# Kernel optimization log

Measured on AMD Instinct MI355X. Metric: run time of the kernel, lower is better.

Reference implementation:

```python
import jax, jax.numpy as jnp
import numpy as np

B, S, D, H = 2, 2048, 1024, 16
DK = D // H  # 64

def setup_inputs() -> dict:
    key = jax.random.key(0)
    ks = jax.random.split(key, 12)
    scale = 1.0 / np.sqrt(D)
    return {
        "q": jax.random.normal(ks[0], (B, S, D), jnp.float32),
        "k": jax.random.normal(ks[1], (B, S, D), jnp.float32),
        "v": jax.random.normal(ks[2], (B, S, D), jnp.float32),
        "Wq": jax.random.normal(ks[3], (D, D), jnp.float32) * scale,
        "bq": jnp.zeros((D,), jnp.float32),
        "Wk": jax.random.normal(ks[4], (D, D), jnp.float32) * scale,
        "bk": jnp.zeros((D,), jnp.float32),
        "Wv": jax.random.normal(ks[5], (D, D), jnp.float32) * scale,
        "bv": jnp.zeros((D,), jnp.float32),
        "Wo": jax.random.normal(ks[6], (D, D), jnp.float32) * scale,
        "bo": jnp.zeros((D,), jnp.float32),
        "mask": jnp.ones((B, 1, S, S), jnp.bool_),
    }

def reference(q, k, v, Wq, bq, Wk, bk, Wv, bv, Wo, bo, mask):
    # Linear projections: y = x @ W^T + b (torch nn.Linear convention)
    def proj(x, W, b):
        return x @ W.T + b
    # [B,S,D] -> [B,H,S,DK]
    def split_heads(x):
        return x.reshape(B, S, H, DK).transpose(0, 2, 1, 3)

    query = split_heads(proj(q, Wq, bq))
    key_ = split_heads(proj(k, Wk, bk))
    value = split_heads(proj(v, Wv, bv))

    # NOTE: original uses out-of-place masked_fill whose result is discarded,
    # so mask has no effect on the computation (reproduced faithfully here).
    scores = jnp.einsum('bhqd,bhkd->bhqk', query, key_) / jnp.sqrt(
        jnp.asarray(DK, query.dtype))
    attn = jax.nn.softmax(scores, axis=-1)  # dropout p=0.0: identity
    x = jnp.einsum('bhqk,bhkd->bhqd', attn, value)
    x = x.transpose(0, 2, 1, 3).reshape(B, S, D)
    return proj(x, Wo, bo)
```

## Files before the change

### kernel.cpp

```cpp
#include <hip/hip_runtime.h>
#include <hip/hip_bf16.h>


typedef __attribute__((ext_vector_type(8))) short bf16x8;
typedef __attribute__((ext_vector_type(4))) float f32x4;
typedef unsigned short u16;
typedef unsigned int u32;

#define MFMA16(a, b, c) __builtin_amdgcn_mfma_f32_16x16x32_bf16(a, b, c, 0, 0, 0)
#define EXP2(x) __builtin_amdgcn_exp2f(x)

static __device__ __forceinline__ u16 f2bf(float f) {
    union { __hip_bfloat16 h; u16 u; } v;
    v.h = __float2bfloat16(f);
    return v.u;
}

static __device__ __forceinline__ u16 f2bf_fast(float f) {
    return (u16)((__float_as_uint(f) + 0x8000u) >> 16);
}

static __device__ __forceinline__ void gload16(const u16* g, u16* l) {
    __builtin_amdgcn_global_load_lds(
        (const __attribute__((address_space(1))) void*)g,
        (__attribute__((address_space(3))) void*)l, 16, 0, 0);
}

static __device__ __forceinline__ void cvt16(float4 f0, float4 f1,
                                             float4 f2, float4 f3, u16* o) {
    o[0]=f2bf(f0.x);  o[1]=f2bf(f0.y);  o[2]=f2bf(f0.z);  o[3]=f2bf(f0.w);
    o[4]=f2bf(f1.x);  o[5]=f2bf(f1.y);  o[6]=f2bf(f1.z);  o[7]=f2bf(f1.w);
    o[8]=f2bf(f2.x);  o[9]=f2bf(f2.y);  o[10]=f2bf(f2.z); o[11]=f2bf(f2.w);
    o[12]=f2bf(f3.x); o[13]=f2bf(f3.y); o[14]=f2bf(f3.z); o[15]=f2bf(f3.w);
}

struct CvtArgs16 { const float* in[16]; u16* out[16]; };

__global__ __launch_bounds__(256)
void cvt_multi(CvtArgs16 a)
{
    const int tsel = blockIdx.x >> 9;
    const int i = (((blockIdx.x & 511) * 256) + threadIdx.x) * 8;
    const float* in = a.in[tsel];
    u16* out = a.out[tsel];
    float4 x = *(const float4*)(in + i);
    float4 y = *(const float4*)(in + i + 4);
    u16 o[8];
    o[0]=f2bf(x.x); o[1]=f2bf(x.y); o[2]=f2bf(x.z); o[3]=f2bf(x.w);
    o[4]=f2bf(y.x); o[5]=f2bf(y.y); o[6]=f2bf(y.z); o[7]=f2bf(y.w);
    *(uint4*)(out + i) = *(uint4*)o;
}

struct GemmArgs {
    const float* F[3]; const u16* Wb[3]; const float* bias[3];
    u16* C[3]; float osc[3]; int epi[3];
};

__global__ __launch_bounds__(256)
void gemm_qkv(GemmArgs g)
{
    __shared__ u16 lds_a[2][128 * 32];
    __shared__ u16 lds_b[2][128 * 32];

    const int z = blockIdx.y;
    const float* Fp = g.F[z];
    const u16*  Gp = g.Wb[z];
    const int epi = g.epi[z];

    const int t    = threadIdx.x;
    const int lane = t & 63;
    const int w    = t >> 6;
    const int wm   = w >> 1, wn = w & 1;
    const int ll   = lane & 15;
    const int lg   = lane >> 4;

    const int bx  = blockIdx.x;
    const int swz = (bx & 7) * 32 + (bx >> 3);
    const int tile_m = (epi == 1 ? (swz & 7) : (swz >> 3)) * 128;
    const int tile_n = (epi == 1 ? (swz >> 3) : (swz & 7)) * 128;

    const int rowF = (epi == 1) ? tile_n : tile_m;
    const int rowG = (epi == 1) ? tile_m : tile_n;

    const int c0   = w * 2;
    const int lrow = lane >> 2;
    const int lcol = (lane & 3) * 8;

    const int srow = t >> 1;
    const int scol = (t & 1) * 16;
    const float* Fbase = Fp + (size_t)(rowF + srow) * 1024 + scol;
    const u16*   Gb0   = Gp + (size_t)(rowG + c0 * 16 + lrow) * 1024 + lcol;

    f32x4 acc[4][4] = {};

    {
        u16* ldsG = (epi == 1) ? lds_a[0] : lds_b[0];
        #pragma unroll
        for (int j = 0; j < 2; j++)
            gload16(Gb0 + (size_t)j * 16 * 1024, &ldsG[(c0 + j) * 512]);

        float4 f0 = *(const float4*)(Fbase);
        float4 f1 = *(const float4*)(Fbase + 4);
        float4 f2 = *(const float4*)(Fbase + 8);
        float4 f3 = *(const float4*)(Fbase + 12);
        u16 tmp[16];
        cvt16(f0, f1, f2, f3, tmp);
        u16* ldsF = (epi == 1) ? lds_b[0] : lds_a[0];
        *(uint4*)&ldsF[srow * 32 + scol]     = *(uint4*)tmp;
        *(uint4*)&ldsF[srow * 32 + scol + 8] = *(uint4*)(tmp + 8);
    }
    __syncthreads();

    int cur = 0;
    for (int kt = 0; kt < 1024; kt += 32) {
        const int nxt = cur ^ 1;
        const bool more = (kt + 32 < 1024);

        float4 f0, f1, f2, f3;
        if (more) {
            const float* Fs = Fbase + kt + 32;
            f0 = *(const float4*)(Fs);
            f1 = *(const float4*)(Fs + 4);
            f2 = *(const float4*)(Fs + 8);
            f3 = *(const float4*)(Fs + 12);
            u16* ldsG = (epi == 1) ? lds_a[nxt] : lds_b[nxt];
            #pragma unroll
            for (int j = 0; j < 2; j++)
                gload16(Gb0 + (size_t)j * 16 * 1024 + kt + 32,
                        &ldsG[(c0 + j) * 512]);
        }

        bf16x8 af[4], bfr[4];
        #pragma unroll
        for (int i = 0; i < 4; i++)
            af[i] = *(bf16x8*)&lds_a[cur][(wm * 64 + i * 16 + ll) * 32 + lg * 8];
        #pragma unroll
        for (int j = 0; j < 4; j++)
            bfr[j] = *(bf16x8*)&lds_b[cur][(wn * 64 + j * 16 + ll) * 32 + lg * 8];
        #pragma unroll
        for (int i = 0; i < 4; i++)
            #pragma unroll
            for (int j = 0; j < 4; j++)
                acc[i][j] = MFMA16(af[i], bfr[j], acc[i][j]);

        if (more) {
            u16 tmp[16];
            cvt16(f0, f1, f2, f3, tmp);
            u16* ldsF = (epi == 1) ? lds_b[nxt] : lds_a[nxt];
            *(uint4*)&ldsF[srow * 32 + scol]     = *(uint4*)tmp;
            *(uint4*)&ldsF[srow * 32 + scol + 8] = *(uint4*)(tmp + 8);
        }

        __syncthreads();
        cur = nxt;
    }

    const float osc = g.osc[z];
    const float* bias = g.bias[z];
    u16* Cp = g.C[z];

    #pragma unroll
    for (int i = 0; i < 4; i++) {
        const int row0 = tile_m + wm * 64 + i * 16 + lg * 4;
        #pragma unroll
        for (int j = 0; j < 4; j++) {
            const int col = tile_n + wn * 64 + j * 16 + ll;
            if (epi == 1) {
                const int b = col >> 11, s = col & 2047;
                #pragma unroll
                for (int r = 0; r < 4; r++)
                    Cp[(size_t)(b * 1024 + row0 + r) * 2048 + s] =
                        f2bf(acc[i][j][r] + bias[row0 + r]);
            } else {
                const float bias_v = bias[col];
                const int h = col >> 6, dk = col & 63;
                const int b = row0 >> 11;
                #pragma unroll
                for (int r = 0; r < 4; r++) {
                    const int s = (row0 + r) & 2047;
                    Cp[((size_t)(b * 16 + h) * 2048 + s) * 64 + dk] =
                        f2bf((acc[i][j][r] + bias_v) * osc);
                }
            }
        }
    }
}

__global__ __launch_bounds__(256)
void gemm_out(const u16* __restrict__ Ap, const u16* __restrict__ Wp,
              const float* __restrict__ bias, float* __restrict__ Cp)
{
    __shared__ u16 lds_a[2][128 * 32];
    __shared__ u16 lds_b[2][64 * 32];

    const int t    = threadIdx.x;
    const int lane = t & 63;
    const int w    = t >> 6;
    const int wm   = w >> 1, wn = w & 1;
    const int ll   = lane & 15;
    const int lg   = lane >> 4;

    const int bx  = blockIdx.x;
    const int swz = (bx & 7) * 64 + (bx >> 3);
    const int tile_m = (swz >> 4) * 128;
    const int tile_n = (swz & 15) * 64;

    const int lrow = lane >> 2;
    const int lcol = (lane & 3) * 8;

    f32x4 acc[4][2] = {};

    #define OSTAGE(buf, kt)                                                    \
    {                                                                          \
        _Pragma("unroll")                                                      \
        for (int j = 0; j < 3; j++) {                                          \
            const int c = w * 3 + j;                                           \
            if (c < 8) {                                                       \
                const int row = tile_m + c * 16 + lrow;                        \
                const int col = (kt) + lcol;                                   \
                const u16* ga = Ap + ((size_t)((row >> 11) * 16 + (col >> 6))  \
                                      * 2048 + (row & 2047)) * 64 + (col & 63);\
                gload16(ga, &lds_a[buf][c * 512]);                             \
            } else {                                                           \
                const int cc = c - 8;                                          \
                gload16(Wp + (size_t)(tile_n + cc * 16 + lrow) * 1024          \
                        + (kt) + lcol, &lds_b[buf][cc * 512]);                 \
            }                                                                  \
        }                                                                      \
    }

    OSTAGE(0, 0);
    __syncthreads();

    int cur = 0;
    for (int kt = 0; kt < 1024; kt += 32) {
        if (kt + 32 < 1024) OSTAGE(cur ^ 1, kt + 32);

        bf16x8 af[4], bfr[2];
        #pragma unroll
        for (int i = 0; i < 4; i++)
            af[i] = *(bf16x8*)&lds_a[cur][(wm * 64 + i * 16 + ll) * 32 + lg * 8];
        #pragma unroll
        for (int j = 0; j < 2; j++)
            bfr[j] = *(bf16x8*)&lds_b[cur][(wn * 32 + j * 16 + ll) * 32 + lg * 8];
        #pragma unroll
        for (int i = 0; i < 4; i++)
            #pragma unroll
            for (int j = 0; j < 2; j++)
                acc[i][j] = MFMA16(af[i], bfr[j], acc[i][j]);

        __syncthreads();
        cur ^= 1;
    }
    #undef OSTAGE

    #pragma unroll
    for (int i = 0; i < 4; i++) {
        const int row0 = tile_m + wm * 64 + i * 16 + lg * 4;
        #pragma unroll
        for (int j = 0; j < 2; j++) {
            const int col = tile_n + wn * 32 + j * 16 + ll;
            const float bias_v = bias[col];
            #pragma unroll
            for (int r = 0; r < 4; r++)
                Cp[(size_t)(row0 + r) * 1024 + col] = acc[i][j][r] + bias_v;
        }
    }
}

__global__ __launch_bounds__(512)
void attn_kernel(const u16* __restrict__ Qh, const u16* __restrict__ Kh,
                 const u16* __restrict__ Vt, u16* __restrict__ Oh)
{
    __shared__ u16 lds_k[2][64 * 64];
    __shared__ u16 lds_v[2][64 * 64];
    __shared__ u16 lds_p[8][16 * 64];

    const int t    = threadIdx.x;
    const int lane = t & 63;
    const int w    = t >> 6;
    const int ll   = lane & 15;
    const int lg   = lane >> 4;
    const int r7   = ll & 7;

    const int bx  = blockIdx.x;
    const int swz = (bx & 7) * 64 + (bx >> 3);
    const int qt = swz & 15;
    const int bh = swz >> 4;
    const int q0 = qt * 128 + w * 16;

    const u16* Qbase = Qh + ((size_t)bh * 2048 + q0 + ll) * 64 + lg * 8;
    const bf16x8 bq0 = *(const bf16x8*)(Qbase);
    const bf16x8 bq1 = *(const bf16x8*)(Qbase + 32);

    bf16x8 bones;
    #pragma unroll
    for (int i = 0; i < 8; i++) bones[i] = (short)0x3F80;

    f32x4 acc[4] = {};
    f32x4 acc_l = {};

    const int srow = lane >> 3;
    const int scol = 8 * ((lane & 7) ^ srow);
    const u16* Kg = Kh + (size_t)bh * 2048 * 64;
    const u16* Vg = Vt + (size_t)bh * 64 * 2048;

    #define ASTAGE(buf, kt)                                                    \
    {                                                                          \
        const int rr = w * 8 + srow;                                           \
        gload16(Kg + (size_t)((kt) + rr) * 64 + scol, &lds_k[buf][w * 512]);   \
        gload16(Vg + (size_t)rr * 2048 + (kt) + scol, &lds_v[buf][w * 512]);   \
    }

    ASTAGE(0, 0);
    __syncthreads();

    u16* lp = lds_p[w];
    int cur = 0;

    for (int kt = 0; kt < 2048; kt += 64) {
        if (kt + 64 < 2048) ASTAGE(cur ^ 1, kt + 64);

        f32x4 s[4];
        __builtin_amdgcn_s_setprio(1);
        #pragma unroll
        for (int ks = 0; ks < 4; ks++) {
            const u16* kp = &lds_k[cur][(ks * 16 + ll) * 64];
            const bf16x8 ak0 = *(const bf16x8*)(kp + ((lg * 8)      ^ (r7 * 8)));
            const bf16x8 ak1 = *(const bf16x8*)(kp + ((lg * 8 + 32) ^ (r7 * 8)));
            f32x4 z = {0.f, 0.f, 0.f, 0.f};
            z = MFMA16(ak0, bq0, z);
            z = MFMA16(ak1, bq1, z);
            s[ks] = z;
        }
        __builtin_amdgcn_s_setprio(0);

        #pragma unroll
        for (int ks = 0; ks < 4; ks++) {
            u16 pk[4];
            #pragma unroll
            for (int r = 0; r < 4; r++) pk[r] = f2bf_fast(EXP2(s[ks][r]));
            *(uint2*)&lp[ll * 64 + ((ks * 16 + lg * 4) ^ (r7 * 8))] = *(uint2*)pk;
        }

        __builtin_amdgcn_s_setprio(1);
        #pragma unroll
        for (int ks2 = 0; ks2 < 2; ks2++) {
            const int so = (ks2 * 32 + lg * 8) ^ (r7 * 8);
            const bf16x8 pa = *(const bf16x8*)&lp[ll * 64 + so];
            #pragma unroll
            for (int dt = 0; dt < 4; dt++) {
                const bf16x8 bv = *(const bf16x8*)&lds_v[cur][(dt * 16 + ll) * 64 + so];
                acc[dt] = MFMA16(pa, bv, acc[dt]);
            }
            acc_l = MFMA16(pa, bones, acc_l);
        }
        __builtin_amdgcn_s_setprio(0);

        __syncthreads();
        cur ^= 1;
    }
    #undef ASTAGE

    #pragma unroll
    for (int r = 0; r < 4; r++) {
        const float lq = 1.f / acc_l[r];
        const int qg = q0 + lg * 4 + r;
        u16* Op = Oh + ((size_t)bh * 2048 + qg) * 64 + ll;
        #pragma unroll
        for (int dt = 0; dt < 4; dt++)
            Op[dt * 16] = f2bf(acc[dt][r] * lq);
    }
}

extern "C" void kernel_launch(void* const* d_in, const int* in_sizes, int n_in,
                              void* d_out, int out_size, void* d_ws, size_t ws_size,
                              hipStream_t stream) {
    const float* q  = (const float*)d_in[0];
    const float* k  = (const float*)d_in[1];
    const float* v  = (const float*)d_in[2];
    const float* Wq = (const float*)d_in[3];
    const float* bq = (const float*)d_in[4];
    const float* Wk = (const float*)d_in[5];
    const float* bk = (const float*)d_in[6];
    const float* Wv = (const float*)d_in[7];
    const float* bv = (const float*)d_in[8];
    const float* Wo = (const float*)d_in[9];
    const float* bo = (const float*)d_in[10];
    float* out = (float*)d_out;

    const size_t M4 = (size_t)4 * 1024 * 1024;
    const size_t M1 = (size_t)1024 * 1024;
    const float qscale = 0.18033688011112042f;
    const dim3 blk(256);

    u16* Qh  = (u16*)d_ws;
    u16* Kh  = Qh + M4;
    u16* Vtb = Kh + M4;
    u16* Oh  = Vtb + M4;
    u16* Wqb = Oh + M4;
    u16* Wkb = Wqb + M1;
    u16* Wvb = Wkb + M1;
    u16* Wob = Wvb + M1;

    CvtArgs16 cv;
    for (int j = 0; j < 16; j++) { cv.in[j] = Wq; cv.out[j] = Wqb; }
    cv.in[0]=Wq; cv.out[0]=Wqb;
    cv.in[1]=Wk; cv.out[1]=Wkb;
    cv.in[2]=Wv; cv.out[2]=Wvb;
    cv.in[3]=Wo; cv.out[3]=Wob;
    cvt_multi<<<4 * 512, blk, 0, stream>>>(cv);

    GemmArgs ga;
    ga.F[0]=q;   ga.F[1]=k;   ga.F[2]=v;
    ga.Wb[0]=Wqb; ga.Wb[1]=Wkb; ga.Wb[2]=Wvb;
    ga.bias[0]=bq; ga.bias[1]=bk; ga.bias[2]=bv;
    ga.C[0]=Qh; ga.C[1]=Kh; ga.C[2]=Vtb;
    ga.osc[0]=qscale; ga.osc[1]=1.0f; ga.osc[2]=1.0f;
    ga.epi[0]=3; ga.epi[1]=3; ga.epi[2]=1;
    gemm_qkv<<<dim3(256, 3), blk, 0, stream>>>(ga);

    attn_kernel<<<512, dim3(512), 0, stream>>>(Qh, Kh, Vtb, Oh);

    gemm_out<<<512, blk, 0, stream>>>(Oh, Wob, bo, out);
}
```

Before: 122.2 us.

## Switch attention kernel to 32x32 MFMA tiles with 4 waves of 32 query rows

Rewrites the attention inner loop to use 32x32x16 bf16 MFMA instead of 16x16x32. Each wave now owns 32 query rows and the block drops from 8 waves to 4 (blk, presumably 256 threads). K/V staging is redistributed so each wave loads twice as many rows, and the P tile and output layout are remapped to the 32x32 accumulator layout. The aim is fewer MFMA and LDS-read instructions per unit of work and more register reuse. The cost is higher register pressure and fewer waves per block to hide latency.

```diff
diff --git a/kernel.cpp b/kernel.cpp
--- a/kernel.cpp
+++ b/kernel.cpp
@@ -2,12 +2,14 @@
 #include <hip/hip_bf16.h>
 
 
-typedef __attribute__((ext_vector_type(8))) short bf16x8;
-typedef __attribute__((ext_vector_type(4))) float f32x4;
+typedef __attribute__((ext_vector_type(8)))  short bf16x8;
+typedef __attribute__((ext_vector_type(4)))  float f32x4;
+typedef __attribute__((ext_vector_type(16))) float f32x16;
 typedef unsigned short u16;
 typedef unsigned int u32;
 
 #define MFMA16(a, b, c) __builtin_amdgcn_mfma_f32_16x16x32_bf16(a, b, c, 0, 0, 0)
+#define MFMA32(a, b, c) __builtin_amdgcn_mfma_f32_32x32x16_bf16(a, b, c, 0, 0, 0)
 #define EXP2(x) __builtin_amdgcn_exp2f(x)
 
 static __device__ __forceinline__ u16 f2bf(float f) {
@@ -268,37 +270,37 @@
     }
 }
 
-__global__ __launch_bounds__(512)
+__global__ __launch_bounds__(256)
 void attn_kernel(const u16* __restrict__ Qh, const u16* __restrict__ Kh,
                  const u16* __restrict__ Vt, u16* __restrict__ Oh)
 {
     __shared__ u16 lds_k[2][64 * 64];
     __shared__ u16 lds_v[2][64 * 64];
-    __shared__ u16 lds_p[8][16 * 64];
+    __shared__ u16 lds_p[4][32 * 64];
 
     const int t    = threadIdx.x;
     const int lane = t & 63;
     const int w    = t >> 6;
-    const int ll   = lane & 15;
-    const int lg   = lane >> 4;
-    const int r7   = ll & 7;
+    const int ll32 = lane & 31;
+    const int hi   = lane >> 5;
 
     const int bx  = blockIdx.x;
     const int swz = (bx & 7) * 64 + (bx >> 3);
     const int qt = swz & 15;
     const int bh = swz >> 4;
-    const int q0 = qt * 128 + w * 16;
-
-    const u16* Qbase = Qh + ((size_t)bh * 2048 + q0 + ll) * 64 + lg * 8;
-    const bf16x8 bq0 = *(const bf16x8*)(Qbase);
-    const bf16x8 bq1 = *(const bf16x8*)(Qbase + 32);
+    const int q0 = qt * 128 + w * 32;
+
+    const u16* Qb = Qh + ((size_t)bh * 2048 + q0 + ll32) * 64 + hi * 8;
+    bf16x8 bq[4];
+    #pragma unroll
+    for (int c = 0; c < 4; c++) bq[c] = *(const bf16x8*)(Qb + c * 16);
 
     bf16x8 bones;
     #pragma unroll
     for (int i = 0; i < 8; i++) bones[i] = (short)0x3F80;
 
-    f32x4 acc[4] = {};
-    f32x4 acc_l = {};
+    f32x16 o32[2] = {};
+    f32x16 accl  = {};
 
     const int srow = lane >> 3;
     const int scol = 8 * ((lane & 7) ^ srow);
@@ -307,9 +309,15 @@
 
     #define ASTAGE(buf, kt)                                                    \
     {                                                                          \
-        const int rr = w * 8 + srow;                                           \
-        gload16(Kg + (size_t)((kt) + rr) * 64 + scol, &lds_k[buf][w * 512]);   \
-        gload16(Vg + (size_t)rr * 2048 + (kt) + scol, &lds_v[buf][w * 512]);   \
+        const int rr = w * 16 + srow;                                          \
+        gload16(Kg + (size_t)((kt) + rr) * 64 + scol,                          \
+                &lds_k[buf][w * 1024]);                                        \
+        gload16(Kg + (size_t)((kt) + rr + 8) * 64 + scol,                      \
+                &lds_k[buf][w * 1024 + 512]);                                  \
+        gload16(Vg + (size_t)rr * 2048 + (kt) + scol,                          \
+                &lds_v[buf][w * 1024]);                                        \
+        gload16(Vg + (size_t)(rr + 8) * 2048 + (kt) + scol,                    \
+                &lds_v[buf][w * 1024 + 512]);                                  \
     }
 
     ASTAGE(0, 0);
@@ -321,39 +329,48 @@
     for (int kt = 0; kt < 2048; kt += 64) {
         if (kt + 64 < 2048) ASTAGE(cur ^ 1, kt + 64);
 
-        f32x4 s[4];
+        f32x16 s32[2];
         __builtin_amdgcn_s_setprio(1);
         #pragma unroll
-        for (int ks = 0; ks < 4; ks++) {
-            const u16* kp = &lds_k[cur][(ks * 16 + ll) * 64];
-            const bf16x8 ak0 = *(const bf16x8*)(kp + ((lg * 8)      ^ (r7 * 8)));
-            const bf16x8 ak1 = *(const bf16x8*)(kp + ((lg * 8 + 32) ^ (r7 * 8)));
-            f32x4 z = {0.f, 0.f, 0.f, 0.f};
-            z = MFMA16(ak0, bq0, z);
-            z = MFMA16(ak1, bq1, z);
-            s[ks] = z;
+        for (int kb = 0; kb < 2; kb++) {
+            f32x16 z = {};
+            #pragma unroll
+            for (int c = 0; c < 4; c++) {
+                const int r = kb * 32 + ll32;
+                const bf16x8 ak = *(const bf16x8*)
+                    &lds_k[cur][r * 64 + (((c * 2 + hi) ^ (r & 7)) * 8)];
+                z = MFMA32(ak, bq[c], z);
+            }
+            s32[kb] = z;
         }
         __builtin_amdgcn_s_setprio(0);
 
         #pragma unroll
-        for (int ks = 0; ks < 4; ks++) {
-            u16 pk[4];
-            #pragma unroll
-            for (int r = 0; r < 4; r++) pk[r] = f2bf_fast(EXP2(s[ks][r]));
-            *(uint2*)&lp[ll * 64 + ((ks * 16 + lg * 4) ^ (r7 * 8))] = *(uint2*)pk;
+        for (int kb = 0; kb < 2; kb++) {
+            #pragma unroll
+            for (int j = 0; j < 4; j++) {
+                u16 pk[4];
+                #pragma unroll
+                for (int rr = 0; rr < 4; rr++)
+                    pk[rr] = f2bf_fast(EXP2(s32[kb][j * 4 + rr]));
+                *(uint2*)&lp[ll32 * 64 + (((kb * 4 + j) ^ (ll32 & 7)) * 8)
+                             + 4 * hi] = *(uint2*)pk;
+            }
         }
 
         __builtin_amdgcn_s_setprio(1);
         #pragma unroll
-        for (int ks2 = 0; ks2 < 2; ks2++) {
-            const int so = (ks2 * 32 + lg * 8) ^ (r7 * 8);
-            const bf16x8 pa = *(const bf16x8*)&lp[ll * 64 + so];
-            #pragma unroll
-            for (int dt = 0; dt < 4; dt++) {
-                const bf16x8 bv = *(const bf16x8*)&lds_v[cur][(dt * 16 + ll) * 64 + so];
-                acc[dt] = MFMA16(pa, bv, acc[dt]);
+        for (int kc = 0; kc < 4; kc++) {
+            const bf16x8 pa = *(const bf16x8*)
+                &lp[ll32 * 64 + (((kc * 2 + hi) ^ (ll32 & 7)) * 8)];
+            #pragma unroll
+            for (int db = 0; db < 2; db++) {
+                const int r = db * 32 + ll32;
+                const bf16x8 bv = *(const bf16x8*)
+                    &lds_v[cur][r * 64 + (((kc * 2 + hi) ^ (r & 7)) * 8)];
+                o32[db] = MFMA32(pa, bv, o32[db]);
             }
-            acc_l = MFMA16(pa, bones, acc_l);
+            accl = MFMA32(pa, bones, accl);
         }
         __builtin_amdgcn_s_setprio(0);
 
@@ -363,13 +380,12 @@
     #undef ASTAGE
 
     #pragma unroll
-    for (int r = 0; r < 4; r++) {
-        const float lq = 1.f / acc_l[r];
-        const int qg = q0 + lg * 4 + r;
-        u16* Op = Oh + ((size_t)bh * 2048 + qg) * 64 + ll;
-        #pragma unroll
-        for (int dt = 0; dt < 4; dt++)
-            Op[dt * 16] = f2bf(acc[dt][r] * lq);
+    for (int r = 0; r < 16; r++) {
+        const float lq = 1.f / accl[r];
+        const int qg = q0 + (r & 3) + 8 * (r >> 2) + 4 * hi;
+        u16* Op = Oh + ((size_t)bh * 2048 + qg) * 64 + ll32;
+        Op[0]  = f2bf(o32[0][r] * lq);
+        Op[32] = f2bf(o32[1][r] * lq);
     }
 }
 
@@ -420,7 +436,7 @@
     ga.epi[0]=3; ga.epi[1]=3; ga.epi[2]=1;
     gemm_qkv<<<dim3(256, 3), blk, 0, stream>>>(ga);
 
-    attn_kernel<<<512, dim3(512), 0, stream>>>(Qh, Kh, Vtb, Oh);
+    attn_kernel<<<512, blk, 0, stream>>>(Qh, Kh, Vtb, Oh);
 
     gemm_out<<<512, blk, 0, stream>>>(Oh, Wob, bo, out);
 }
```

Measured after the change: 130.7 us. 1.07x slower.
